# Kernel tuning notes

Measured on AMD Instinct MI355X. Metric: run time of the kernel, lower is better.

## Reference

```python
import jax, jax.numpy as jnp
import numpy as np

B = 4
NS = [65536, 16384, 4096, 1024, 256]   # nodes per mesh level
DEG = 16                               # avg degree
KORD = 6                               # Chebyshev polynomial order
FE = [3, 16, 16, 16, 32]               # encoder filters
FD = [32, 16, 16, 16, 16, 3]           # decoder filters
Z = 64                                 # latent dim


def cheb_norm(edge_index, n):
    # symmetric normalization D^-1/2 A D^-1/2 per ChebConv_Coma.norm
    row, col = edge_index
    deg = jnp.zeros((n,), jnp.float32).at[row].add(jnp.ones(row.shape, jnp.float32))
    dis = jnp.where(deg > 0, deg ** -0.5, 0.0)
    return dis[row] * dis[col]


def propagate(x, row, col, norm):
    # out[b, row] += norm * x[b, col]   (sparse adjacency matvec, batched)
    return jnp.zeros_like(x).at[:, row].add(x[:, col] * norm[None, :, None])


def cheb_conv(x, edge_index, norm, W, b):
    # Chebyshev recursion: T0 = x, T1 = L x, Tk = 2 L T_{k-1} - T_{k-2}
    row, col = edge_index
    Tx0 = x
    out = jnp.einsum('bnf,fg->bng', Tx0, W[0])
    Tx1 = propagate(x, row, col, norm)
    out = out + jnp.einsum('bnf,fg->bng', Tx1, W[1])
    for k in range(2, W.shape[0]):
        Tx2 = 2.0 * propagate(Tx1, row, col, norm) - Tx0
        out = out + jnp.einsum('bnf,fg->bng', Tx2, W[k])
        Tx0, Tx1 = Tx1, Tx2
    return out + b if b is not None else out


def pool(x, idx, w):
    # sparse pooling matmul: 3 nnz per output row; idx/w: [Nout, 3]
    return jnp.einsum('bnkf,nk->bnf', x[:, idx], w)


def coma_forward(x, eis, dids, dws, uids, uws, encW, encB, decW, decB,
                 enc_w, enc_b, dec_w, dec_b):
    norms = [cheb_norm(eis[i], NS[i]) for i in range(5)]
    h = x.reshape(B, NS[0], FE[0])
    # encoder: cheb conv + relu + downsample pool, 4 levels
    for i in range(4):
        h = jax.nn.relu(cheb_conv(h, eis[i], norms[i], encW[i], encB[i]))
        h = pool(h, dids[i], dws[i])
    h = h.reshape(B, NS[-1] * FE[-1])
    z = jax.nn.relu(h @ enc_w + enc_b)
    # decoder
    h = jax.nn.relu(z @ dec_w + dec_b).reshape(B, NS[-1], FD[0])
    for i in range(4):
        lvl = 3 - i
        h = pool(h, uids[lvl], uws[lvl])
        h = jax.nn.relu(cheb_conv(h, eis[lvl], norms[lvl], decW[i], decB[i]))
    h = cheb_conv(h, eis[0], norms[0], decW[4], None)  # last conv, no bias
    return h.reshape(-1, FE[0])


def setup_inputs() -> dict:
    key = jax.random.key(0)
    ks = iter(jax.random.split(key, 80))
    inp = {}
    inp['x'] = jax.random.normal(next(ks), (B * NS[0], FE[0]), jnp.float32)
    for i, n in enumerate(NS):
        inp[f'ei{i}'] = jax.random.randint(next(ks), (2, DEG * n), 0, n)
    for i in range(4):
        inp[f'down_i{i}'] = jax.random.randint(next(ks), (NS[i + 1], 3), 0, NS[i])
        inp[f'down_w{i}'] = jax.random.uniform(next(ks), (NS[i + 1], 3), jnp.float32)
        inp[f'up_i{i}'] = jax.random.randint(next(ks), (NS[i], 3), 0, NS[i + 1])
        inp[f'up_w{i}'] = jax.random.uniform(next(ks), (NS[i], 3), jnp.float32)
    for i in range(4):
        inp[f'ew{i}'] = 0.1 * jax.random.normal(next(ks), (KORD, FE[i], FE[i + 1]), jnp.float32)
        inp[f'eb{i}'] = jnp.zeros((FE[i + 1],), jnp.float32)
    for i in range(5):
        inp[f'dw{i}'] = 0.1 * jax.random.normal(next(ks), (KORD, FD[i], FD[i + 1]), jnp.float32)
    for i in range(4):
        inp[f'db{i}'] = jnp.zeros((FD[i + 1],), jnp.float32)
    inp['enc_w'] = 0.1 * jax.random.normal(next(ks), (NS[-1] * FE[-1], Z), jnp.float32)
    inp['enc_b'] = 0.1 * jnp.ones((Z,), jnp.float32)
    inp['dec_w'] = 0.1 * jax.random.normal(next(ks), (Z, FD[0] * NS[-1]), jnp.float32)
    inp['dec_b'] = 0.1 * jnp.ones((FD[0] * NS[-1],), jnp.float32)
    return inp


def reference(x, ei0, ei1, ei2, ei3, ei4,
              down_i0, down_w0, up_i0, up_w0,
              down_i1, down_w1, up_i1, up_w1,
              down_i2, down_w2, up_i2, up_w2,
              down_i3, down_w3, up_i3, up_w3,
              ew0, eb0, ew1, eb1, ew2, eb2, ew3, eb3,
              dw0, dw1, dw2, dw3, dw4, db0, db1, db2, db3,
              enc_w, enc_b, dec_w, dec_b):
    eis = [ei0, ei1, ei2, ei3, ei4]
    dids = [down_i0, down_i1, down_i2, down_i3]
    dws = [down_w0, down_w1, down_w2, down_w3]
    uids = [up_i0, up_i1, up_i2, up_i3]
    uws = [up_w0, up_w1, up_w2, up_w3]
    encW = [ew0, ew1, ew2, ew3]
    encB = [eb0, eb1, eb2, eb3]
    decW = [dw0, dw1, dw2, dw3, dw4]
    decB = [db0, db1, db2, db3]
    return coma_forward(x, eis, dids, dws, uids, uws, encW, encB, decW, decB,
                        enc_w, enc_b, dec_w, dec_b)
```

## Files before the change

### kernel.cpp

```cpp
#include <hip/hip_runtime.h>

#define TPB 256

static constexpr int B_ = 4;
static constexpr int DEG_ = 16;

using u16 = unsigned short;

static constexpr int LB0 = 0, LB1 = 65536, LB2 = 81920, LB3 = 86016, LB4 = 87040;
static constexpr int CE0 = 0, CE1 = 1048576, CE2 = 1310720, CE3 = 1376256, CE4 = 1392640;


__device__ inline float b2f(u16 u) { return __uint_as_float((unsigned)u << 16); }
__device__ inline u16 f2b(float f) {
    unsigned b = __float_as_uint(f);
    b += 0x7fffu + ((b >> 16) & 1u);
    return (u16)(b >> 16);
}

template<int F>
__device__ inline void load_row_bf16(const u16* __restrict__ p, float* v) {
    if constexpr (F % 8 == 0) {
        #pragma unroll
        for (int i = 0; i < F / 8; ++i) {
            uint4 raw = reinterpret_cast<const uint4*>(p)[i];
            unsigned rr[4] = {raw.x, raw.y, raw.z, raw.w};
            #pragma unroll
            for (int k = 0; k < 4; ++k) {
                v[i * 8 + 2 * k]     = __uint_as_float(rr[k] << 16);
                v[i * 8 + 2 * k + 1] = __uint_as_float(rr[k] & 0xffff0000u);
            }
        }
    } else {
        #pragma unroll
        for (int f = 0; f < F; ++f) v[f] = b2f(p[f]);
    }
}

template<int F>
__device__ inline void store_row_bf16(u16* __restrict__ p, const float* v) {
    if constexpr (F % 8 == 0) {
        #pragma unroll
        for (int i = 0; i < F / 8; ++i) {
            uint4 raw;
            unsigned* rr = &raw.x;
            #pragma unroll
            for (int k = 0; k < 4; ++k)
                rr[k] = (unsigned)f2b(v[i * 8 + 2 * k]) |
                        ((unsigned)f2b(v[i * 8 + 2 * k + 1]) << 16);
            reinterpret_cast<uint4*>(p)[i] = raw;
        }
    } else {
        #pragma unroll
        for (int f = 0; f < F; ++f) p[f] = f2b(v[f]);
    }
}


__global__ void cnt_kernel(const int* __restrict__ row, int* __restrict__ cnt, int E) {
    int e = blockIdx.x * blockDim.x + threadIdx.x;
    if (e < E) atomicAdd(&cnt[row[e]], 1);
}

__global__ void dis_kernel(const int* __restrict__ cnt, float* __restrict__ dis, int n) {
    int i = blockIdx.x * blockDim.x + threadIdx.x;
    if (i < n) dis[i] = cnt[i] > 0 ? rsqrtf((float)cnt[i]) : 0.f;
}

__global__ void scanA_kernel(const int* __restrict__ cnt, int* __restrict__ partial,
                             int* __restrict__ bsum) {
    __shared__ int sdata[256];
    int tid = threadIdx.x;
    int base = blockIdx.x * 1024 + tid * 4;
    int v0 = cnt[base], v1 = cnt[base + 1], v2 = cnt[base + 2], v3 = cnt[base + 3];
    int tsum = v0 + v1 + v2 + v3;
    sdata[tid] = tsum;
    __syncthreads();
    for (int ofs = 1; ofs < 256; ofs <<= 1) {
        int x = (tid >= ofs) ? sdata[tid - ofs] : 0;
        __syncthreads();
        sdata[tid] += x;
        __syncthreads();
    }
    int excl = sdata[tid] - tsum;
    partial[base] = excl;         excl += v0;
    partial[base + 1] = excl;     excl += v1;
    partial[base + 2] = excl;     excl += v2;
    partial[base + 3] = excl;
    if (tid == 255) bsum[blockIdx.x] = sdata[255];
}

__global__ void scanB_kernel(int* __restrict__ bsum, int nb) {
    __shared__ int s[128];
    int tid = threadIdx.x;
    int v = tid < nb ? bsum[tid] : 0;
    s[tid] = v;
    __syncthreads();
    for (int ofs = 1; ofs < 128; ofs <<= 1) {
        int x = (tid >= ofs) ? s[tid - ofs] : 0;
        __syncthreads();
        s[tid] += x;
        __syncthreads();
    }
    if (tid < nb) bsum[tid] = s[tid] - v;
}

__global__ void scanC_kernel(const int* __restrict__ partial, const int* __restrict__ bsum,
                             int* __restrict__ rp0, int* __restrict__ rp1,
                             int* __restrict__ rp2, int* __restrict__ rp3) {
    int i = blockIdx.x * blockDim.x + threadIdx.x;
    if (i >= LB4) return;
    int g = partial[i] + bsum[i >> 10];
    if (i < LB1)      rp0[i - LB0] = g - CE0;
    else if (i < LB2) rp1[i - LB1] = g - CE1;
    else if (i < LB3) rp2[i - LB2] = g - CE2;
    else              rp3[i - LB3] = g - CE3;
    if (i == 0) {
        rp0[LB1 - LB0] = CE1 - CE0;
        rp1[LB2 - LB1] = CE2 - CE1;
        rp2[LB3 - LB2] = CE3 - CE2;
        rp3[LB4 - LB3] = CE4 - CE3;
    }
}

__global__ void fill_kernel(const int* __restrict__ row, const int* __restrict__ col,
                            const int* __restrict__ rowptr, int* __restrict__ cur,
                            u16* __restrict__ ccol, int E) {
    int e = blockIdx.x * blockDim.x + threadIdx.x;
    if (e >= E) return;
    int r = row[e];
    int pos = rowptr[r] + atomicAdd(&cur[r], 1);
    ccol[pos] = (u16)col[e];
}


__global__ void f2b_tr_kernel(const float* __restrict__ in, u16* __restrict__ out, int N) {
    int t = blockIdx.x * blockDim.x + threadIdx.x;
    if (t >= B_ * N * 3) return;
    int f = t % 3;
    int nb = t / 3;
    int b = nb & 3;
    int n = nb >> 2;
    out[t] = f2b(in[((size_t)b * N + n) * 3 + f]);
}

template<int F, bool FIRST>
__global__ __launch_bounds__(128) void sweep_k(
    const u16* __restrict__ gsrc, const u16* __restrict__ selfp, u16* __restrict__ dst,
    const int* __restrict__ rowptr, const u16* __restrict__ ccol,
    const float* __restrict__ dis, int N)
{
    int t = blockIdx.x * 128 + (int)threadIdx.x;
    if (t >= B_ * N) return;
    int r = t >> 2;
    int b = t & 3;

    float tv[F];
    if constexpr (FIRST) {
        #pragma unroll
        for (int f = 0; f < F; ++f) tv[f] = 0.f;
    } else {
        float sv[F];
        load_row_bf16<F>(selfp + (size_t)t * F, sv);
        #pragma unroll
        for (int f = 0; f < F; ++f) tv[f] = -sv[f];
    }
    const float scale = (FIRST ? 1.0f : 2.0f) * dis[r];
    int beg = rowptr[r], end = rowptr[r + 1];
    for (int j = beg; j < end; ++j) {
        int c = (int)ccol[j];
        float w = scale * dis[c];
        float gv[F];
        load_row_bf16<F>(gsrc + (size_t)((c << 2) | b) * F, gv);
        #pragma unroll
        for (int f = 0; f < F; ++f) tv[f] += w * gv[f];
    }
    store_row_bf16<F>(dst + (size_t)t * F, tv);
}

template<int F, int G, bool OSTD>
__global__ __launch_bounds__(128) void combine_k(
    const u16* __restrict__ T0, const u16* __restrict__ T1, const u16* __restrict__ T2,
    const u16* __restrict__ T3, const u16* __restrict__ T4, const u16* __restrict__ T5,
    const float* __restrict__ W6, const float* __restrict__ bias,
    u16* __restrict__ outb, float* __restrict__ outf, int N, int relu)
{
    __shared__ float sW[6 * F * G];
    for (int i = threadIdx.x; i < 6 * F * G; i += 128) sW[i] = W6[i];
    __syncthreads();
    int t = blockIdx.x * 128 + (int)threadIdx.x;
    if (t >= B_ * N) return;

    float acc[G];
    #pragma unroll
    for (int g = 0; g < G; ++g) acc[g] = 0.f;

    const u16* Ts[6] = {T0, T1, T2, T3, T4, T5};
    #pragma unroll
    for (int k = 0; k < 6; ++k) {
        float tv[F];
        load_row_bf16<F>(Ts[k] + (size_t)t * F, tv);
        const float* w = sW + k * F * G;
        #pragma unroll
        for (int f = 0; f < F; ++f) {
            float x = tv[f];
            #pragma unroll
            for (int g = 0; g < G; ++g) acc[g] += x * w[f * G + g];
        }
    }
    if (bias) {
        #pragma unroll
        for (int g = 0; g < G; ++g) acc[g] += bias[g];
    }
    if (relu) {
        #pragma unroll
        for (int g = 0; g < G; ++g) acc[g] = fmaxf(acc[g], 0.f);
    }
    if (OSTD) {
        int r = t >> 2, b = t & 3;
        float* orow = outf + ((size_t)b * N + r) * G;
        #pragma unroll
        for (int g = 0; g < G; ++g) orow[g] = acc[g];
    } else {
        store_row_bf16<G>(outb + (size_t)t * G, acc);
    }
}


__global__ void pool_kernel(const u16* __restrict__ in, u16* __restrict__ out,
                            const int* __restrict__ idx, const float* __restrict__ w,
                            int Nout, int F) {
    int t = blockIdx.x * blockDim.x + threadIdx.x;
    if (t >= B_ * Nout * F) return;
    int f = t % F;
    int nb = t / F;
    int b = nb & 3;
    int n = nb >> 2;
    float acc = 0.f;
    for (int k = 0; k < 3; ++k) {
        int src = idx[n * 3 + k];
        acc += w[n * 3 + k] * b2f(in[(size_t)((src << 2) | b) * F + f]);
    }
    out[t] = f2b(acc);
}

__global__ void dense_enc_kernel(const u16* __restrict__ h, const float* __restrict__ W,
                                 const float* __restrict__ bias, float* __restrict__ z) {
    int b = blockIdx.x >> 6;
    int g = blockIdx.x & 63;
    int tid = threadIdx.x;
    float acc = 0.f;
    for (int i = tid; i < 8192; i += 256) {
        int n = i >> 5, f = i & 31;
        acc += b2f(h[(((size_t)n << 2) | b) * 32 + f]) * W[(size_t)i * 64 + g];
    }
    __shared__ float red[256];
    red[tid] = acc;
    __syncthreads();
    for (int sft = 128; sft > 0; sft >>= 1) {
        if (tid < sft) red[tid] += red[tid + sft];
        __syncthreads();
    }
    if (tid == 0) z[b * 64 + g] = fmaxf(red[0] + bias[g], 0.f);
}

__global__ void dense_dec_kernel(const float* __restrict__ z, const float* __restrict__ W,
                                 const float* __restrict__ bias, u16* __restrict__ out) {
    int t = blockIdx.x * blockDim.x + threadIdx.x;
    if (t >= B_ * 8192) return;
    int b = t / 8192, j = t % 8192;
    float acc = bias[j];
    for (int k = 0; k < 64; ++k) acc += z[b * 64 + k] * W[(size_t)k * 8192 + j];
    int n = j >> 5, f = j & 31;
    out[(((size_t)n << 2) | b) * 32 + f] = f2b(fmaxf(acc, 0.f));
}


static inline unsigned cdivu(size_t a, size_t b) { return (unsigned)((a + b - 1) / b); }

template<int F, int G, bool OSTD = false>
static void run_cheb(const u16* X, u16* const* T, const float* Wk, const float* bias,
                     int relu, u16* outb, float* outf,
                     const int* rp, const u16* cc, const float* dis, int N, hipStream_t s) {
    unsigned g = (unsigned)((size_t)B_ * N / 128);
    sweep_k<F, true><<<g, 128, 0, s>>>(X, nullptr, T[0], rp, cc, dis, N);
    sweep_k<F, false><<<g, 128, 0, s>>>(T[0], X, T[1], rp, cc, dis, N);
    sweep_k<F, false><<<g, 128, 0, s>>>(T[1], T[0], T[2], rp, cc, dis, N);
    sweep_k<F, false><<<g, 128, 0, s>>>(T[2], T[1], T[3], rp, cc, dis, N);
    sweep_k<F, false><<<g, 128, 0, s>>>(T[3], T[2], T[4], rp, cc, dis, N);
    combine_k<F, G, OSTD><<<g, 128, 0, s>>>(X, T[0], T[1], T[2], T[3], T[4],
                                            Wk, bias, outb, outf, N, relu);
}

extern "C" void kernel_launch(void* const* d_in, const int* in_sizes, int n_in,
                              void* d_out, int out_size, void* d_ws, size_t ws_size,
                              hipStream_t stream) {
    (void)in_sizes; (void)n_in; (void)out_size; (void)ws_size;
    hipStream_t s = stream;

    static const int NS_[5] = {65536, 16384, 4096, 1024, 256};
    static const int LBa[5] = {LB0, LB1, LB2, LB3, LB4};
    static const int CEa[5] = {CE0, CE1, CE2, CE3, CE4};

    const float* x = (const float*)d_in[0];
    const int* ei[4];
    for (int l = 0; l < 4; ++l) ei[l] = (const int*)d_in[1 + l];
    const int* down_i[4]; const float* down_w[4];
    const int* up_i[4];   const float* up_w[4];
    for (int i = 0; i < 4; ++i) {
        down_i[i] = (const int*)d_in[6 + 4 * i];
        down_w[i] = (const float*)d_in[7 + 4 * i];
        up_i[i]   = (const int*)d_in[8 + 4 * i];
        up_w[i]   = (const float*)d_in[9 + 4 * i];
    }
    const float* encW[4]; const float* encB[4];
    for (int i = 0; i < 4; ++i) {
        encW[i] = (const float*)d_in[22 + 2 * i];
        encB[i] = (const float*)d_in[23 + 2 * i];
    }
    const float* decW[5];
    for (int i = 0; i < 5; ++i) decW[i] = (const float*)d_in[30 + i];
    const float* decB[4];
    for (int i = 0; i < 4; ++i) decB[i] = (const float*)d_in[35 + i];
    const float* enc_w = (const float*)d_in[39];
    const float* enc_b = (const float*)d_in[40];
    const float* dec_w = (const float*)d_in[41];
    const float* dec_b = (const float*)d_in[42];

    float* ws = (float*)d_ws;
    size_t off = 0;
    const size_t HSLOT = (size_t)B_ * 65536 * 16 / 2;
    u16* XA = (u16*)(ws + off); off += HSLOT;
    u16* XBuf = (u16*)(ws + off); off += HSLOT;
    u16* T[5];
    for (int i = 0; i < 5; ++i) { T[i] = (u16*)(ws + off); off += HSLOT; }
    int* cntAll = (int*)(ws + off); off += LB4;
    int* curAll = (int*)(ws + off); off += LB4;
    int* partial = (int*)(ws + off); off += LB4;
    int* bsum = (int*)(ws + off); off += 128;
    float* disAll = ws + off; off += LB4;
    int* rowptr[4];
    for (int l = 0; l < 4; ++l) { rowptr[l] = (int*)(ws + off); off += (size_t)NS_[l] + 4; }
    u16* ccolAll = (u16*)(ws + off); off += (CE4 + 1) / 2;
    float* zbuf = ws + off; off += 256;

    hipMemsetAsync(cntAll, 0, (size_t)LB4 * sizeof(int), s);
    hipMemsetAsync(curAll, 0, (size_t)LB4 * sizeof(int), s);
    for (int l = 0; l < 4; ++l) {
        int E = DEG_ * NS_[l];
        cnt_kernel<<<cdivu(E, TPB), TPB, 0, s>>>(ei[l], cntAll + LBa[l], E);
    }
    dis_kernel<<<cdivu(LB4, TPB), TPB, 0, s>>>(cntAll, disAll, LB4);
    scanA_kernel<<<85, 256, 0, s>>>(cntAll, partial, bsum);
    scanB_kernel<<<1, 128, 0, s>>>(bsum, 85);
    scanC_kernel<<<cdivu(LB4, TPB), TPB, 0, s>>>(partial, bsum,
                                                 rowptr[0], rowptr[1], rowptr[2], rowptr[3]);
    for (int l = 0; l < 4; ++l) {
        int E = DEG_ * NS_[l];
        fill_kernel<<<cdivu(E, TPB), TPB, 0, s>>>(ei[l], ei[l] + E, rowptr[l],
                                                  curAll + LBa[l], ccolAll + CEa[l], E);
    }

    const float* dis[4]; const u16* cc[4];
    for (int l = 0; l < 4; ++l) { dis[l] = disAll + LBa[l]; cc[l] = ccolAll + CEa[l]; }

    f2b_tr_kernel<<<cdivu((size_t)B_ * 65536 * 3, TPB), TPB, 0, s>>>(x, XA, 65536);
    run_cheb<3, 16>(XA, T, encW[0], encB[0], 1, XBuf, nullptr,
                    rowptr[0], cc[0], dis[0], NS_[0], s);
    pool_kernel<<<cdivu((size_t)B_ * NS_[1] * 16, TPB), TPB, 0, s>>>(
        XBuf, XA, down_i[0], down_w[0], NS_[1], 16);
    run_cheb<16, 16>(XA, T, encW[1], encB[1], 1, XBuf, nullptr,
                     rowptr[1], cc[1], dis[1], NS_[1], s);
    pool_kernel<<<cdivu((size_t)B_ * NS_[2] * 16, TPB), TPB, 0, s>>>(
        XBuf, XA, down_i[1], down_w[1], NS_[2], 16);
    run_cheb<16, 16>(XA, T, encW[2], encB[2], 1, XBuf, nullptr,
                     rowptr[2], cc[2], dis[2], NS_[2], s);
    pool_kernel<<<cdivu((size_t)B_ * NS_[3] * 16, TPB), TPB, 0, s>>>(
        XBuf, XA, down_i[2], down_w[2], NS_[3], 16);
    run_cheb<16, 32>(XA, T, encW[3], encB[3], 1, XBuf, nullptr,
                     rowptr[3], cc[3], dis[3], NS_[3], s);
    pool_kernel<<<cdivu((size_t)B_ * NS_[4] * 32, TPB), TPB, 0, s>>>(
        XBuf, XA, down_i[3], down_w[3], NS_[4], 32);

    dense_enc_kernel<<<B_ * 64, 256, 0, s>>>(XA, enc_w, enc_b, zbuf);
    dense_dec_kernel<<<cdivu((size_t)B_ * 8192, TPB), TPB, 0, s>>>(zbuf, dec_w, dec_b, XBuf);

    pool_kernel<<<cdivu((size_t)B_ * NS_[3] * 32, TPB), TPB, 0, s>>>(
        XBuf, XA, up_i[3], up_w[3], NS_[3], 32);
    run_cheb<32, 16>(XA, T, decW[0], decB[0], 1, XBuf, nullptr,
                     rowptr[3], cc[3], dis[3], NS_[3], s);
    pool_kernel<<<cdivu((size_t)B_ * NS_[2] * 16, TPB), TPB, 0, s>>>(
        XBuf, XA, up_i[2], up_w[2], NS_[2], 16);
    run_cheb<16, 16>(XA, T, decW[1], decB[1], 1, XBuf, nullptr,
                     rowptr[2], cc[2], dis[2], NS_[2], s);
    pool_kernel<<<cdivu((size_t)B_ * NS_[1] * 16, TPB), TPB, 0, s>>>(
        XBuf, XA, up_i[1], up_w[1], NS_[1], 16);
    run_cheb<16, 16>(XA, T, decW[2], decB[2], 1, XBuf, nullptr,
                     rowptr[1], cc[1], dis[1], NS_[1], s);
    pool_kernel<<<cdivu((size_t)B_ * NS_[0] * 16, TPB), TPB, 0, s>>>(
        XBuf, XA, up_i[0], up_w[0], NS_[0], 16);
    run_cheb<16, 16>(XA, T, decW[3], decB[3], 1, XBuf, nullptr,
                     rowptr[0], cc[0], dis[0], NS_[0], s);
    run_cheb<16, 3, true>(XBuf, T, decW[4], nullptr, 0, nullptr, (float*)d_out,
                          rowptr[0], cc[0], dis[0], NS_[0], s);
}
```

Before: 1.136 ms.

## Fuse last Chebyshev sweep into combine and split level-0 features into halves

Folds the fifth propagation sweep into the combine kernel, so T5 is computed per row and multiplied by its weight slice directly without being written to and reread from memory. For the two largest-level decoder convolutions (65536 nodes, 16 features), features are split into two 8-channel planes, and the sweeps run separately on each half. Each neighbour gather then touches a smaller row, which may improve cache hit rates, at the cost of twice as many sweep launches and index reads. Workspace buffers are reorganised into lo/hi planes to support this.

Result: slower. 2.109 ms (+85.6%).

```diff
diff --git a/kernel.cpp b/kernel.cpp
--- a/kernel.cpp
+++ b/kernel.cpp
@@ -178,26 +178,29 @@
     store_row_bf16<F>(dst + (size_t)t * F, tv);
 }
 
-template<int F, int G, bool OSTD>
-__global__ __launch_bounds__(128) void combine_k(
-    const u16* __restrict__ T0, const u16* __restrict__ T1, const u16* __restrict__ T2,
-    const u16* __restrict__ T3, const u16* __restrict__ T4, const u16* __restrict__ T5,
-    const float* __restrict__ W6, const float* __restrict__ bias,
-    u16* __restrict__ outb, float* __restrict__ outf, int N, int relu)
+template<int F, int G>
+__global__ __launch_bounds__(128) void combine_fused(
+    const u16* __restrict__ X, const u16* __restrict__ T1, const u16* __restrict__ T2,
+    const u16* __restrict__ T3, const u16* __restrict__ T4,
+    const int* __restrict__ rowptr, const u16* __restrict__ ccol,
+    const float* __restrict__ dis, const float* __restrict__ W6,
+    const float* __restrict__ bias, u16* __restrict__ out, int N, int relu)
 {
     __shared__ float sW[6 * F * G];
     for (int i = threadIdx.x; i < 6 * F * G; i += 128) sW[i] = W6[i];
     __syncthreads();
     int t = blockIdx.x * 128 + (int)threadIdx.x;
     if (t >= B_ * N) return;
+    int r = t >> 2;
+    int b = t & 3;
 
     float acc[G];
     #pragma unroll
     for (int g = 0; g < G; ++g) acc[g] = 0.f;
 
-    const u16* Ts[6] = {T0, T1, T2, T3, T4, T5};
+    const u16* Ts[5] = {X, T1, T2, T3, T4};
     #pragma unroll
-    for (int k = 0; k < 6; ++k) {
+    for (int k = 0; k < 5; ++k) {
         float tv[F];
         load_row_bf16<F>(Ts[k] + (size_t)t * F, tv);
         const float* w = sW + k * F * G;
@@ -208,6 +211,74 @@
             for (int g = 0; g < G; ++g) acc[g] += x * w[f * G + g];
         }
     }
+    {
+        float tv[F];
+        load_row_bf16<F>(T3 + (size_t)t * F, tv);
+        #pragma unroll
+        for (int f = 0; f < F; ++f) tv[f] = -tv[f];
+        const float scale = 2.0f * dis[r];
+        int beg = rowptr[r], end = rowptr[r + 1];
+        for (int j = beg; j < end; ++j) {
+            int c = (int)ccol[j];
+            float w = scale * dis[c];
+            float gv[F];
+            load_row_bf16<F>(T4 + (size_t)((c << 2) | b) * F, gv);
+            #pragma unroll
+            for (int f = 0; f < F; ++f) tv[f] += w * gv[f];
+        }
+        const float* w5 = sW + 5 * F * G;
+        #pragma unroll
+        for (int f = 0; f < F; ++f) {
+            float x = tv[f];
+            #pragma unroll
+            for (int g = 0; g < G; ++g) acc[g] += x * w5[f * G + g];
+        }
+    }
+    if (bias) {
+        #pragma unroll
+        for (int g = 0; g < G; ++g) acc[g] += bias[g];
+    }
+    if (relu) {
+        #pragma unroll
+        for (int g = 0; g < G; ++g) acc[g] = fmaxf(acc[g], 0.f);
+    }
+    store_row_bf16<G>(out + (size_t)t * G, acc);
+}
+
+template<int G, bool OSTD>
+__global__ __launch_bounds__(128) void combine_split(
+    const u16* __restrict__ Xlo, const u16* __restrict__ Xhi,
+    const u16* __restrict__ Tlo, const u16* __restrict__ Thi,
+    const float* __restrict__ W6, const float* __restrict__ bias,
+    u16* __restrict__ outLo, u16* __restrict__ outHi,
+    float* __restrict__ outF, int N, int relu)
+{
+    __shared__ float sW[6 * 16 * G];
+    for (int i = threadIdx.x; i < 6 * 16 * G; i += 128) sW[i] = W6[i];
+    __syncthreads();
+    int t = blockIdx.x * 128 + (int)threadIdx.x;
+    if (t >= B_ * N) return;
+    const size_t PL = (size_t)N * B_ * 8;
+
+    float acc[G];
+    #pragma unroll
+    for (int g = 0; g < G; ++g) acc[g] = 0.f;
+
+    #pragma unroll
+    for (int k = 0; k < 6; ++k) {
+        const u16* plo = (k == 0) ? Xlo : Tlo + (size_t)(k - 1) * PL;
+        const u16* phi = (k == 0) ? Xhi : Thi + (size_t)(k - 1) * PL;
+        float tv[16];
+        load_row_bf16<8>(plo + (size_t)t * 8, tv);
+        load_row_bf16<8>(phi + (size_t)t * 8, tv + 8);
+        const float* w = sW + k * 16 * G;
+        #pragma unroll
+        for (int f = 0; f < 16; ++f) {
+            float x = tv[f];
+            #pragma unroll
+            for (int g = 0; g < G; ++g) acc[g] += x * w[f * G + g];
+        }
+    }
     if (bias) {
         #pragma unroll
         for (int g = 0; g < G; ++g) acc[g] += bias[g];
@@ -218,11 +289,12 @@
     }
     if (OSTD) {
         int r = t >> 2, b = t & 3;
-        float* orow = outf + ((size_t)b * N + r) * G;
+        float* orow = outF + ((size_t)b * N + r) * G;
         #pragma unroll
         for (int g = 0; g < G; ++g) orow[g] = acc[g];
     } else {
-        store_row_bf16<G>(outb + (size_t)t * G, acc);
+        store_row_bf16<8>(outLo + (size_t)t * 8, acc);
+        store_row_bf16<8>(outHi + (size_t)t * 8, acc + 8);
     }
 }
 
@@ -244,6 +316,24 @@
     out[t] = f2b(acc);
 }
 
+__global__ void pool_split_kernel(const u16* __restrict__ in, u16* __restrict__ outLo,
+                                  u16* __restrict__ outHi, const int* __restrict__ idx,
+                                  const float* __restrict__ w, int Nout) {
+    int t = blockIdx.x * blockDim.x + threadIdx.x;
+    if (t >= B_ * Nout * 16) return;
+    int f = t % 16;
+    int nb = t / 16;
+    int b = nb & 3;
+    int n = nb >> 2;
+    float acc = 0.f;
+    for (int k = 0; k < 3; ++k) {
+        int src = idx[n * 3 + k];
+        acc += w[n * 3 + k] * b2f(in[(size_t)((src << 2) | b) * 16 + f]);
+    }
+    u16* dst = (f < 8) ? outLo : outHi;
+    dst[(size_t)((n << 2) | b) * 8 + (f & 7)] = f2b(acc);
+}
+
 __global__ void dense_enc_kernel(const u16* __restrict__ h, const float* __restrict__ W,
                                  const float* __restrict__ bias, float* __restrict__ z) {
     int b = blockIdx.x >> 6;
@@ -278,18 +368,37 @@
 
 static inline unsigned cdivu(size_t a, size_t b) { return (unsigned)((a + b - 1) / b); }
 
-template<int F, int G, bool OSTD = false>
+template<int F, int G>
 static void run_cheb(const u16* X, u16* const* T, const float* Wk, const float* bias,
-                     int relu, u16* outb, float* outf,
+                     int relu, u16* out,
                      const int* rp, const u16* cc, const float* dis, int N, hipStream_t s) {
     unsigned g = (unsigned)((size_t)B_ * N / 128);
     sweep_k<F, true><<<g, 128, 0, s>>>(X, nullptr, T[0], rp, cc, dis, N);
     sweep_k<F, false><<<g, 128, 0, s>>>(T[0], X, T[1], rp, cc, dis, N);
     sweep_k<F, false><<<g, 128, 0, s>>>(T[1], T[0], T[2], rp, cc, dis, N);
     sweep_k<F, false><<<g, 128, 0, s>>>(T[2], T[1], T[3], rp, cc, dis, N);
-    sweep_k<F, false><<<g, 128, 0, s>>>(T[3], T[2], T[4], rp, cc, dis, N);
-    combine_k<F, G, OSTD><<<g, 128, 0, s>>>(X, T[0], T[1], T[2], T[3], T[4],
-                                            Wk, bias, outb, outf, N, relu);
+    combine_fused<F, G><<<g, 128, 0, s>>>(X, T[0], T[1], T[2], T[3],
+                                          rp, cc, dis, Wk, bias, out, N, relu);
+}
+
+template<int G, bool OSTD>
+static void run_cheb_split(const u16* Xlo, const u16* Xhi, u16* TL, u16* TH, size_t PL,
+                           const float* Wk, const float* bias, int relu,
+                           u16* outLo, u16* outHi, float* outF,
+                           const int* rp, const u16* cc, const float* dis,
+                           int N, hipStream_t s) {
+    unsigned g = (unsigned)((size_t)B_ * N / 128);
+    for (int h = 0; h < 2; ++h) {
+        const u16* X = h ? Xhi : Xlo;
+        u16* T = h ? TH : TL;
+        sweep_k<8, true><<<g, 128, 0, s>>>(X, nullptr, T, rp, cc, dis, N);
+        sweep_k<8, false><<<g, 128, 0, s>>>(T, X, T + PL, rp, cc, dis, N);
+        sweep_k<8, false><<<g, 128, 0, s>>>(T + PL, T, T + 2 * PL, rp, cc, dis, N);
+        sweep_k<8, false><<<g, 128, 0, s>>>(T + 2 * PL, T + PL, T + 3 * PL, rp, cc, dis, N);
+        sweep_k<8, false><<<g, 128, 0, s>>>(T + 3 * PL, T + 2 * PL, T + 4 * PL, rp, cc, dis, N);
+    }
+    combine_split<G, OSTD><<<g, 128, 0, s>>>(Xlo, Xhi, TL, TH, Wk, bias,
+                                             outLo, outHi, outF, N, relu);
 }
 
 extern "C" void kernel_launch(void* const* d_in, const int* in_sizes, int n_in,
@@ -329,11 +438,19 @@
 
     float* ws = (float*)d_ws;
     size_t off = 0;
-    const size_t HSLOT = (size_t)B_ * 65536 * 16 / 2;
-    u16* XA = (u16*)(ws + off); off += HSLOT;
-    u16* XBuf = (u16*)(ws + off); off += HSLOT;
-    u16* T[5];
-    for (int i = 0; i < 5; ++i) { T[i] = (u16*)(ws + off); off += HSLOT; }
+    const size_t PLANEF = 1048576;
+    const size_t PL = 2 * PLANEF;
+    u16* XPlo = (u16*)(ws + off); off += PLANEF;
+    u16* XPhi = (u16*)(ws + off); off += PLANEF;
+    u16* YPlo = (u16*)(ws + off); off += PLANEF;
+    u16* YPhi = (u16*)(ws + off); off += PLANEF;
+    u16* TL = (u16*)(ws + off); off += 5 * PLANEF;
+    u16* TH = (u16*)(ws + off); off += 5 * PLANEF;
+    u16* XA = XPlo;
+    u16* XB = YPlo;
+    u16* Tf[4];
+    for (int k = 0; k < 4; ++k) Tf[k] = TL + (size_t)k * PL;
+
     int* cntAll = (int*)(ws + off); off += LB4;
     int* curAll = (int*)(ws + off); off += LB4;
     int* partial = (int*)(ws + off); off += LB4;
@@ -365,42 +482,44 @@
     for (int l = 0; l < 4; ++l) { dis[l] = disAll + LBa[l]; cc[l] = ccolAll + CEa[l]; }
 
     f2b_tr_kernel<<<cdivu((size_t)B_ * 65536 * 3, TPB), TPB, 0, s>>>(x, XA, 65536);
-    run_cheb<3, 16>(XA, T, encW[0], encB[0], 1, XBuf, nullptr,
+    run_cheb<3, 16>(XA, Tf, encW[0], encB[0], 1, XB,
                     rowptr[0], cc[0], dis[0], NS_[0], s);
     pool_kernel<<<cdivu((size_t)B_ * NS_[1] * 16, TPB), TPB, 0, s>>>(
-        XBuf, XA, down_i[0], down_w[0], NS_[1], 16);
-    run_cheb<16, 16>(XA, T, encW[1], encB[1], 1, XBuf, nullptr,
+        XB, XA, down_i[0], down_w[0], NS_[1], 16);
+    run_cheb<16, 16>(XA, Tf, encW[1], encB[1], 1, XB,
                      rowptr[1], cc[1], dis[1], NS_[1], s);
     pool_kernel<<<cdivu((size_t)B_ * NS_[2] * 16, TPB), TPB, 0, s>>>(
-        XBuf, XA, down_i[1], down_w[1], NS_[2], 16);
-    run_cheb<16, 16>(XA, T, encW[2], encB[2], 1, XBuf, nullptr,
+        XB, XA, down_i[1], down_w[1], NS_[2], 16);
+    run_cheb<16, 16>(XA, Tf, encW[2], encB[2], 1, XB,
                      rowptr[2], cc[2], dis[2], NS_[2], s);
     pool_kernel<<<cdivu((size_t)B_ * NS_[3] * 16, TPB), TPB, 0, s>>>(
-        XBuf, XA, down_i[2], down_w[2], NS_[3], 16);
-    run_cheb<16, 32>(XA, T, encW[3], encB[3], 1, XBuf, nullptr,
+        XB, XA, down_i[2], down_w[2], NS_[3], 16);
+    run_cheb<16, 32>(XA, Tf, encW[3], encB[3], 1, XB,
                      rowptr[3], cc[3], dis[3], NS_[3], s);
     pool_kernel<<<cdivu((size_t)B_ * NS_[4] * 32, TPB), TPB, 0, s>>>(
-        XBuf, XA, down_i[3], down_w[3], NS_[4], 32);
+        XB, XA, down_i[3], down_w[3], NS_[4], 32);
 
     dense_enc_kernel<<<B_ * 64, 256, 0, s>>>(XA, enc_w, enc_b, zbuf);
-    dense_dec_kernel<<<cdivu((size_t)B_ * 8192, TPB), TPB, 0, s>>>(zbuf, dec_w, dec_b, XBuf);
+    dense_dec_kernel<<<cdivu((size_t)B_ * 8192, TPB), TPB, 0, s>>>(zbuf, dec_w, dec_b, XB);
 
     pool_kernel<<<cdivu((size_t)B_ * NS_[3] * 32, TPB), TPB, 0, s>>>(
-        XBuf, XA, up_i[3], up_w[3], NS_[3], 32);
-    run_cheb<32, 16>(XA, T, decW[0], decB[0], 1, XBuf, nullptr,
+        XB, XA, up_i[3], up_w[3], NS_[3], 32);
+    run_cheb<32, 16>(XA, Tf, decW[0], decB[0], 1, XB,
                      rowptr[3], cc[3], dis[3], NS_[3], s);
     pool_kernel<<<cdivu((size_t)B_ * NS_[2] * 16, TPB), TPB, 0, s>>>(
-        XBuf, XA, up_i[2], up_w[2], NS_[2], 16);
-    run_cheb<16, 16>(XA, T, decW[1], decB[1], 1, XBuf, nullptr,
+        XB, XA, up_i[2], up_w[2], NS_[2], 16);
+    run_cheb<16, 16>(XA, Tf, decW[1], decB[1], 1, XB,
                      rowptr[2], cc[2], dis[2], NS_[2], s);
     pool_kernel<<<cdivu((size_t)B_ * NS_[1] * 16, TPB), TPB, 0, s>>>(
-        XBuf, XA, up_i[1], up_w[1], NS_[1], 16);
-    run_cheb<16, 16>(XA, T, decW[2], decB[2], 1, XBuf, nullptr,
+        XB, XA, up_i[1], up_w[1], NS_[1], 16);
+    run_cheb<16, 16>(XA, Tf, decW[2], decB[2], 1, XB,
                      rowptr[1], cc[1], dis[1], NS_[1], s);
-    pool_kernel<<<cdivu((size_t)B_ * NS_[0] * 16, TPB), TPB, 0, s>>>(
-        XBuf, XA, up_i[0], up_w[0], NS_[0], 16);
-    run_cheb<16, 16>(XA, T, decW[3], decB[3], 1, XBuf, nullptr,
-                     rowptr[0], cc[0], dis[0], NS_[0], s);
-    run_cheb<16, 3, true>(XBuf, T, decW[4], nullptr, 0, nullptr, (float*)d_out,
-                          rowptr[0], cc[0], dis[0], NS_[0], s);
-}
+    pool_split_kernel<<<cdivu((size_t)B_ * NS_[0] * 16, TPB), TPB, 0, s>>>(
+        XB, XPlo, XPhi, up_i[0], up_w[0], NS_[0]);
+    run_cheb_split<16, false>(XPlo, XPhi, TL, TH, PL, decW[3], decB[3], 1,
+                              YPlo, YPhi, nullptr,
+                              rowptr[0], cc[0], dis[0], NS_[0], s);
+    run_cheb_split<3, true>(YPlo, YPhi, TL, TH, PL, decW[4], nullptr, 0,
+                            nullptr, nullptr, (float*)d_out,
+                            rowptr[0], cc[0], dis[0], NS_[0], s);
+}
```
